# Kernel optimization log

Measured on AMD Instinct MI355X. Metric: run time of the kernel, lower is better.

The kernel has to match this reference:

```python
import jax, jax.numpy as jnp
import numpy as np
import math

CH_IN = 256
NUM_HEADS = 4
HEAD_CH = 64
NUM_GROUPS = 32
EPS = 1e-5


def setup_inputs() -> dict:
    key = jax.random.key(0)
    ks = jax.random.split(key, 12)
    B, C, H, W = 16, CH_IN, 32, 32
    s_in = 1.0 / math.sqrt(C)  # conv 1x1 fan_in init scale
    s_proj = 1.0 / math.sqrt(NUM_HEADS * HEAD_CH)
    return {
        "x": jax.random.normal(ks[0], (B, C, H, W), dtype=jnp.float32),
        "gamma": jnp.ones((C,), dtype=jnp.float32),
        "beta": jnp.zeros((C,), dtype=jnp.float32),
        # per-head 1x1 convs stacked: [num_heads, head_ch, ch_in]
        "wq": jax.random.normal(ks[1], (NUM_HEADS, HEAD_CH, C), dtype=jnp.float32) * s_in,
        "bq": jax.random.normal(ks[2], (NUM_HEADS, HEAD_CH), dtype=jnp.float32) * s_in,
        "wk": jax.random.normal(ks[3], (NUM_HEADS, HEAD_CH, C), dtype=jnp.float32) * s_in,
        "bk": jax.random.normal(ks[4], (NUM_HEADS, HEAD_CH), dtype=jnp.float32) * s_in,
        "wv": jax.random.normal(ks[5], (NUM_HEADS, HEAD_CH, C), dtype=jnp.float32) * s_in,
        "bv": jax.random.normal(ks[6], (NUM_HEADS, HEAD_CH), dtype=jnp.float32) * s_in,
        # output 1x1 conv: [ch_in, num_heads*head_ch]
        "wproj": jax.random.normal(ks[7], (C, NUM_HEADS * HEAD_CH), dtype=jnp.float32) * s_proj,
        "bproj": jax.random.normal(ks[8], (C,), dtype=jnp.float32) * s_proj,
    }


def group_norm(x, gamma, beta):
    B, C, H, W = x.shape
    xg = x.reshape(B, NUM_GROUPS, C // NUM_GROUPS, H, W)
    mean = xg.mean(axis=(2, 3, 4), keepdims=True)
    var = xg.var(axis=(2, 3, 4), keepdims=True)
    xn = (xg - mean) * jax.lax.rsqrt(var + EPS)
    xn = xn.reshape(B, C, H, W)
    return xn * gamma[None, :, None, None] + beta[None, :, None, None]


def reference(x, gamma, beta, wq, bq, wk, bk, wv, bv, wproj, bproj):
    B, C, H, W = x.shape
    L = H * W
    h = group_norm(x, gamma, beta)
    hf = h.reshape(B, C, L)  # [B, C, L]
    # per-head 1x1 convs as batched channel contractions: [B, n_heads, d, L]
    q = jnp.einsum("bcl,ndc->bndl", hf, wq) + bq[None, :, :, None]
    k = jnp.einsum("bcl,ndc->bndl", hf, wk) + bk[None, :, :, None]
    v = jnp.einsum("bcl,ndc->bndl", hf, wv) + bv[None, :, :, None]
    scale = 1.0 / math.sqrt(HEAD_CH)
    scores = jnp.einsum("bndl,bndm->bnlm", q, k) * scale  # [B, n, L, L]
    attn = jax.nn.softmax(scores, axis=-1)
    out = jnp.einsum("bnlm,bndm->bndl", attn, v)  # [B, n, d, L]
    out = out.reshape(B, NUM_HEADS * HEAD_CH, L)  # concat heads along channels
    proj = jnp.einsum("bel,ce->bcl", out, wproj) + bproj[None, :, None]
    return proj.reshape(B, C, H, W) + x
```

## Files before the change

kernel.cpp:

```cpp
#include <hip/hip_runtime.h>
#include <hip/hip_bf16.h>
#include <stdint.h>


typedef __hip_bfloat16 bf16;
typedef __attribute__((ext_vector_type(8))) short short8;
typedef __attribute__((ext_vector_type(4))) float float4v;
typedef __attribute__((ext_vector_type(16))) float float16v;

#if __has_builtin(__builtin_amdgcn_exp2f)
#define EXP2F(x) __builtin_amdgcn_exp2f(x)
#else
#define EXP2F(x) exp2f(x)
#endif

__device__ __forceinline__ float max3f(float a, float b, float c) {
  return fmaxf(fmaxf(a, b), c);
}

__device__ __forceinline__ int qk_fidx(int d, int l) {
  return ((((l >> 5) * 4 + (d >> 4)) * 64 + ((d >> 3) & 1) * 32 + (l & 31)) << 3) + (d & 7);
}
__device__ __forceinline__ int v_fidx(int d, int l) {
  return (((((((l >> 5) * 2 + (d >> 5)) * 2 + ((l >> 4) & 1)) * 2 + ((l >> 3) & 1)) * 32) + (d & 31)) << 3) + (l & 7);
}

__global__ __launch_bounds__(256) void stats_kernel(const float* __restrict__ x,
    float2* __restrict__ stats) {
  int b = blockIdx.x >> 5, g = blockIdx.x & 31;
  const float* xp = x + (size_t)(b * 256 + g * 8) * 1024;
  float s = 0.f, ss = 0.f;
  for (int i = threadIdx.x; i < 8192; i += 256) {
    float v = xp[i]; s += v; ss += v * v;
  }
  #pragma unroll
  for (int o = 32; o; o >>= 1) { s += __shfl_down(s, o); ss += __shfl_down(ss, o); }
  __shared__ float red[2][4];
  int wid = threadIdx.x >> 6;
  if ((threadIdx.x & 63) == 0) { red[0][wid] = s; red[1][wid] = ss; }
  __syncthreads();
  if (threadIdx.x == 0) {
    s  = red[0][0] + red[0][1] + red[0][2] + red[0][3];
    ss = red[1][0] + red[1][1] + red[1][2] + red[1][3];
    float mean = s * (1.f / 8192.f);
    float var  = ss * (1.f / 8192.f) - mean * mean;
    stats[blockIdx.x] = make_float2(mean, rsqrtf(var + 1e-5f));
  }
}

__global__ __launch_bounds__(256) void gnt_kernel(const float* __restrict__ x,
    const float* __restrict__ gamma, const float* __restrict__ beta,
    const float2* __restrict__ stats, bf16* __restrict__ hT, int b_off) {
  __shared__ float T[64][65];
  int zb = blockIdx.z, b = zb + b_off;
  int c0 = blockIdx.y * 64, l0 = blockIdx.x * 64;
  const float* xb = x + (size_t)b * 262144;
  const float2* st = stats + b * 32;
  int tid = threadIdx.x;
  for (int i = tid; i < 4096; i += 256) {
    int cl = i >> 6, ll = i & 63;
    int c = c0 + cl;
    float2 s2 = st[c >> 3];
    T[cl][ll] = (xb[(size_t)c * 1024 + l0 + ll] - s2.x) * s2.y * gamma[c] + beta[c];
  }
  __syncthreads();
  bf16* hb = hT + (size_t)zb * 262144;
  for (int i = tid; i < 4096; i += 256) {
    int ll = i >> 6, cl = i & 63;
    hb[(size_t)(l0 + ll) * 256 + c0 + cl] = __float2bfloat16(T[cl][ll]);
  }
}

__global__ __launch_bounds__(256) void wpack(const float* __restrict__ wq,
    const float* __restrict__ wk, const float* __restrict__ wv,
    const float* __restrict__ wp, bf16* __restrict__ Wb, bf16* __restrict__ Pb) {
  int i = blockIdx.x * 256 + threadIdx.x;
  if (i < 196608) {
    int r = i >> 8, c = i & 255;
    const float* src = (r < 256) ? wq : (r < 512) ? wk : wv;
    Wb[i] = __float2bfloat16(src[(r & 255) * 256 + c]);
  } else {
    int j = i - 196608;
    Pb[j] = __float2bfloat16(wp[j]);
  }
}

__global__ __launch_bounds__(256) void gemm_qkv_mfma(
    const bf16* __restrict__ hT, const bf16* __restrict__ Wb,
    const float* __restrict__ bq, const float* __restrict__ bk,
    const float* __restrict__ bv,
    bf16* __restrict__ qkv, size_t qkv_bstride) {
  __shared__ bf16 As[128][40];
  __shared__ bf16 Bs[128][40];
  int zb = blockIdx.z;
  int m0 = blockIdx.y * 128, l0 = blockIdx.x * 128;
  const bf16* hb = hT + (size_t)zb * 262144;
  int tid = threadIdx.x, lane = tid & 63, wave = tid >> 6;
  int l16 = lane & 15, quad = lane >> 4;
  int mi0 = (wave & 1) * 4, nj0 = (wave >> 1) * 4;
  float4v acc[4][4];
  #pragma unroll
  for (int i = 0; i < 4; i++)
    #pragma unroll
    for (int j = 0; j < 4; j++) acc[i][j] = (float4v){0.f, 0.f, 0.f, 0.f};

  for (int kc = 0; kc < 8; kc++) {
    __syncthreads();
    #pragma unroll
    for (int it = 0; it < 2; it++) {
      int s = it * 256 + tid;
      int mm = s >> 2, kk = (s & 3) * 8;
      *(short8*)&As[mm][kk] = *(const short8*)&Wb[(size_t)(m0 + mm) * 256 + kc * 32 + kk];
      *(short8*)&Bs[mm][kk] = *(const short8*)&hb[(size_t)(l0 + mm) * 256 + kc * 32 + kk];
    }
    __syncthreads();
    short8 af[4], bfr[4];
    #pragma unroll
    for (int i = 0; i < 4; i++) af[i]  = *(const short8*)&As[(mi0 + i) * 16 + l16][quad * 8];
    #pragma unroll
    for (int j = 0; j < 4; j++) bfr[j] = *(const short8*)&Bs[(nj0 + j) * 16 + l16][quad * 8];
    #pragma unroll
    for (int i = 0; i < 4; i++)
      #pragma unroll
      for (int j = 0; j < 4; j++)
        acc[i][j] = __builtin_amdgcn_mfma_f32_16x16x32_bf16(af[i], bfr[j], acc[i][j], 0, 0, 0);
  }

  bf16* Cp = qkv + (size_t)zb * qkv_bstride;
  int sec = m0 >> 8;
  const float* bptr = (sec == 0) ? bq : (sec == 1) ? bk : bv;
  float osc = (sec == 0) ? 0.125f * 1.4426950408889634f : 1.0f;
  #pragma unroll
  for (int i = 0; i < 4; i++) {
    #pragma unroll
    for (int r = 0; r < 4; r++) {
      int m = m0 + (mi0 + i) * 16 + quad * 4 + r;
      int rr = m & 255;
      float bias = bptr[rr];
      int n = rr >> 6, d = rr & 63;
      if (sec <= 1) {
        bf16* Tp = Cp + sec * 262144 + n * 65536;
        #pragma unroll
        for (int j = 0; j < 4; j++) {
          int l = l0 + (nj0 + j) * 16 + l16;
          Tp[qk_fidx(d, l)] = __float2bfloat16((acc[i][j][r] + bias) * osc);
        }
      } else {
        bf16* Vf = Cp + 524288 + n * 65536;
        #pragma unroll
        for (int j = 0; j < 4; j++) {
          int l = l0 + (nj0 + j) * 16 + l16;
          Vf[v_fidx(d, l)] = __float2bfloat16(acc[i][j][r] + bias);
        }
      }
    }
  }
}

__global__ __launch_bounds__(256) void attn_kernel(
    const bf16* __restrict__ qkv, bf16* __restrict__ oT,
    size_t qkv_bstride, size_t o_bstride) {
  __shared__ __align__(16) float OB[2][2][2176];
  __shared__ float mL[2][2][32], lL[2][2][32];

  int zb, n, gg;
  {
    int f = blockIdx.x + (blockIdx.y << 4) + (blockIdx.z << 6);
    if (gridDim.z == 16) {
      int c = f & 7, r = f >> 3;
      int h = (r >> 4) * 8 + c;
      zb = h >> 2; n = h & 3; gg = r & 15;
    } else {
      zb = blockIdx.z; n = blockIdx.y; gg = blockIdx.x;
    }
  }
  const bf16* base = qkv + (size_t)zb * qkv_bstride;
  const bf16* Qf = base + n * 65536;
  const bf16* Kf = base + 262144 + n * 65536;
  const bf16* Vf = base + 524288 + n * 65536;
  int tid = threadIdx.x;
  int lane = tid & 63, wave = tid >> 6;
  int l31 = lane & 31, hb2 = lane >> 5;
  int qt = wave >> 1, half = wave & 1;
  int g = gg * 2 + qt;
  int q0 = g << 5;

  short8 qb[4];
  #pragma unroll
  for (int ds = 0; ds < 4; ds++)
    qb[ds] = *(const short8*)&Qf[(((g * 4 + ds) << 6) + lane) << 3];

  float m_run = -1e30f, l_run = 0.f;
  float16v oaccT[2];
  #pragma unroll
  for (int dh = 0; dh < 2; dh++)
    #pragma unroll
    for (int r = 0; r < 16; r++) oaccT[dh][r] = 0.f;

  auto swp = [&](unsigned int a, unsigned int b, unsigned int& o0, unsigned int& o1) {
#if __has_builtin(__builtin_amdgcn_permlane32_swap)
    auto rr = __builtin_amdgcn_permlane32_swap((int)a, (int)b, false, false);
    o0 = (unsigned int)rr[0]; o1 = (unsigned int)rr[1];
#else
    unsigned int sa = (unsigned int)__shfl_xor((int)a, 32, 64);
    unsigned int sb = (unsigned int)__shfl_xor((int)b, 32, 64);
    o0 = hb2 ? sb : a;
    o1 = hb2 ? b : sa;
#endif
  };

  int k0 = half << 4;
  for (int kt = k0; kt < k0 + 16; kt++) {
    short8 kf[4];
    #pragma unroll
    for (int ds = 0; ds < 4; ds++)
      kf[ds] = *(const short8*)&Kf[(((kt * 4 + ds) << 6) + lane) << 3];
    short8 vf[2][2];
    #pragma unroll
    for (int dh = 0; dh < 2; dh++)
      #pragma unroll
      for (int s = 0; s < 2; s++)
        vf[dh][s] = *(const short8*)&Vf[((((kt * 2 + dh) * 2 + s) << 6) + lane) << 3];

    float16v sacc;
    #pragma unroll
    for (int r = 0; r < 16; r++) sacc[r] = 0.f;
    #pragma unroll
    for (int ds = 0; ds < 4; ds++)
      sacc = __builtin_amdgcn_mfma_f32_32x32x16_bf16(kf[ds], qb[ds], sacc, 0, 0, 0);

    float a0 = max3f(sacc[0], sacc[1], sacc[2]);
    float a1 = max3f(sacc[3], sacc[4], sacc[5]);
    float a2 = max3f(sacc[6], sacc[7], sacc[8]);
    float a3 = max3f(sacc[9], sacc[10], sacc[11]);
    float a4 = max3f(sacc[12], sacc[13], sacc[14]);
    float cmax = fmaxf(max3f(a0, a1, a2), max3f(a3, a4, sacc[15]));
    cmax = fmaxf(cmax, __shfl_xor(cmax, 32, 64));

    if (__any(cmax > m_run + 8.f)) {
      float mnew = fmaxf(m_run, cmax);
      float alpha = EXP2F(m_run - mnew);
      #pragma unroll
      for (int dh = 0; dh < 2; dh++)
        #pragma unroll
        for (int r = 0; r < 16; r++) oaccT[dh][r] *= alpha;
      l_run *= alpha;
      m_run = mnew;
    }

    float p[16];
    #pragma unroll
    for (int r = 0; r < 16; r++) p[r] = EXP2F(sacc[r] - m_run);
    float s0 = (p[0] + p[1]) + (p[2] + p[3]);
    float s1 = (p[4] + p[5]) + (p[6] + p[7]);
    float s2 = (p[8] + p[9]) + (p[10] + p[11]);
    float s3 = (p[12] + p[13]) + (p[14] + p[15]);
    float psum = (s0 + s1) + (s2 + s3);
    psum += __shfl_xor(psum, 32, 64);
    l_run += psum;

    unsigned int w[8];
    #pragma unroll
    for (int i = 0; i < 8; i++) {
      unsigned int pk;
      asm("v_cvt_pk_bf16_f32 %0, %1, %2" : "=v"(pk) : "v"(p[2 * i]), "v"(p[2 * i + 1]));
      w[i] = pk;
    }
    short8 pb[2];
    {
      unsigned int o0, o1, o2, o3;
      swp(w[0], w[2], o0, o2); swp(w[1], w[3], o1, o3);
      unsigned int* pw = (unsigned int*)&pb[0];
      pw[0] = o0; pw[1] = o1; pw[2] = o2; pw[3] = o3;
      swp(w[4], w[6], o0, o2); swp(w[5], w[7], o1, o3);
      pw = (unsigned int*)&pb[1];
      pw[0] = o0; pw[1] = o1; pw[2] = o2; pw[3] = o3;
    }

    #pragma unroll
    for (int dh = 0; dh < 2; dh++)
      #pragma unroll
      for (int s = 0; s < 2; s++)
        oaccT[dh] = __builtin_amdgcn_mfma_f32_32x32x16_bf16(vf[dh][s], pb[s], oaccT[dh], 0, 0, 0);
  }

  #pragma unroll
  for (int dh = 0; dh < 2; dh++)
    #pragma unroll
    for (int rq = 0; rq < 4; rq++) {
      float4v t = {oaccT[dh][4 * rq], oaccT[dh][4 * rq + 1],
                   oaccT[dh][4 * rq + 2], oaccT[dh][4 * rq + 3]};
      *(float4v*)&OB[half][qt][l31 * 68 + dh * 32 + 8 * rq + 4 * hb2] = t;
    }
  if (hb2 == 0) { mL[half][qt][l31] = m_run; lL[half][qt][l31] = l_run; }
  __syncthreads();

  bf16* op = oT + (size_t)zb * o_bstride + n * 64;
  const float* OA = OB[0][qt];
  const float* OBp = OB[1][qt];
  #pragma unroll
  for (int i = 0; i < 16; i++) {
    int q = (half << 4) + i;
    float mA = mL[0][qt][q], mB = mL[1][qt][q];
    float lA = lL[0][qt][q], lB = lL[1][qt][q];
    float ms = fmaxf(mA, mB);
    float eA = EXP2F(mA - ms), eB = EXP2F(mB - ms);
    float inv = 1.f / (lA * eA + lB * eB);
    float va = OA[q * 68 + lane], vb = OBp[q * 68 + lane];
    float o = (va * eA + vb * eB) * inv;
    op[(size_t)(q0 + q) * 256 + lane] = __float2bfloat16(o);
  }
}

__global__ __launch_bounds__(256) void gemm_proj_mfma(
    const bf16* __restrict__ Pb, const bf16* __restrict__ oT,
    const float* __restrict__ bproj, const float* __restrict__ x,
    float* __restrict__ out, int b_off, size_t o_bstride) {
  __shared__ bf16 As[128][40];
  __shared__ bf16 Bs[128][40];
  int zb = blockIdx.z, b = zb + b_off;
  int m0 = blockIdx.y * 128, l0 = blockIdx.x * 128;
  const bf16* ob = oT + (size_t)zb * o_bstride;
  int tid = threadIdx.x, lane = tid & 63, wave = tid >> 6;
  int l16 = lane & 15, quad = lane >> 4;
  int mi0 = (wave & 1) * 4, nj0 = (wave >> 1) * 4;
  float4v acc[4][4];
  #pragma unroll
  for (int i = 0; i < 4; i++)
    #pragma unroll
    for (int j = 0; j < 4; j++) acc[i][j] = (float4v){0.f, 0.f, 0.f, 0.f};

  for (int kc = 0; kc < 8; kc++) {
    __syncthreads();
    #pragma unroll
    for (int it = 0; it < 2; it++) {
      int s = it * 256 + tid;
      int mm = s >> 2, kk = (s & 3) * 8;
      *(short8*)&As[mm][kk] = *(const short8*)&Pb[(size_t)(m0 + mm) * 256 + kc * 32 + kk];
      *(short8*)&Bs[mm][kk] = *(const short8*)&ob[(size_t)(l0 + mm) * 256 + kc * 32 + kk];
    }
    __syncthreads();
    short8 af[4], bfr[4];
    #pragma unroll
    for (int i = 0; i < 4; i++) af[i]  = *(const short8*)&As[(mi0 + i) * 16 + l16][quad * 8];
    #pragma unroll
    for (int j = 0; j < 4; j++) bfr[j] = *(const short8*)&Bs[(nj0 + j) * 16 + l16][quad * 8];
    #pragma unroll
    for (int i = 0; i < 4; i++)
      #pragma unroll
      for (int j = 0; j < 4; j++)
        acc[i][j] = __builtin_amdgcn_mfma_f32_16x16x32_bf16(af[i], bfr[j], acc[i][j], 0, 0, 0);
  }

  #pragma unroll
  for (int i = 0; i < 4; i++) {
    #pragma unroll
    for (int r = 0; r < 4; r++) {
      int m = m0 + (mi0 + i) * 16 + quad * 4 + r;
      float bias = bproj[m];
      #pragma unroll
      for (int j = 0; j < 4; j++) {
        int l = l0 + (nj0 + j) * 16 + l16;
        size_t idx = (size_t)(b * 256 + m) * 1024 + l;
        out[idx] = acc[i][j][r] + bias + x[idx];
      }
    }
  }
}

extern "C" void kernel_launch(void* const* d_in, const int* in_sizes, int n_in,
                              void* d_out, int out_size, void* d_ws, size_t ws_size,
                              hipStream_t stream) {
  int ix = 0, iga = 1, ibe = 2, iwq = 3, ibq = 4, iwk = 5, ibk = 6,
      iwv = 7, ibv = 8, iwp = 9, ibp = 10;
  if (in_sizes[0] != 4194304) {
    if (in_sizes[10] == 4194304 && in_sizes[1] == 256) {
      ibe = 0; ibk = 1; ibp = 2; ibq = 3; ibv = 4; iga = 5;
      iwk = 6; iwp = 7; iwq = 8; iwv = 9; ix = 10;
    } else if (in_sizes[10] == 4194304 && in_sizes[1] == 65536) {
      ibp = 0; iwp = 1; ibv = 2; iwv = 3; ibk = 4; iwk = 5;
      ibq = 6; iwq = 7; ibe = 8; iga = 9; ix = 10;
    } else {
      for (int i = 0; i < 11; i++) if (in_sizes[i] == 4194304) ix = i;
    }
  }
  const float* x     = (const float*)d_in[ix];
  const float* gamma = (const float*)d_in[iga];
  const float* beta  = (const float*)d_in[ibe];
  const float* wq    = (const float*)d_in[iwq];
  const float* bq    = (const float*)d_in[ibq];
  const float* wk    = (const float*)d_in[iwk];
  const float* bk    = (const float*)d_in[ibk];
  const float* wv    = (const float*)d_in[iwv];
  const float* bv    = (const float*)d_in[ibv];
  const float* wproj = (const float*)d_in[iwp];
  const float* bproj = (const float*)d_in[ibp];
  float* out = (float*)d_out;

  const size_t QKV_B = (size_t)768 * 1024;
  const size_t O_B   = (size_t)256 * 1024;
  char* wsp = (char*)d_ws;
  float2* stats = (float2*)wsp;
  bf16* Wb = (bf16*)(wsp + 8192);
  bf16* Pb = (bf16*)(wsp + 8192 + 393216);
  const size_t HT0 = 8192 + 393216 + 131072;
  size_t full_need = HT0 + (size_t)16 * O_B * 2 + (size_t)16 * QKV_B * 2;

  stats_kernel<<<512, 256, 0, stream>>>(x, stats);
  wpack<<<1024, 256, 0, stream>>>(wq, wk, wv, wproj, Wb, Pb);

  if (ws_size >= full_need) {
    bf16* hT  = (bf16*)(wsp + HT0);
    bf16* qkv = (bf16*)(wsp + HT0 + 16 * O_B * 2);
    bf16* oT  = hT;
    gnt_kernel   <<<dim3(16, 4, 16), 256, 0, stream>>>(x, gamma, beta, stats, hT, 0);
    gemm_qkv_mfma<<<dim3(8, 6, 16), 256, 0, stream>>>(hT, Wb, bq, bk, bv, qkv, QKV_B);
    attn_kernel  <<<dim3(16, 4, 16), 256, 0, stream>>>(qkv, oT, QKV_B, O_B);
    gemm_proj_mfma<<<dim3(8, 2, 16), 256, 0, stream>>>(Pb, oT, bproj, x, out, 0, O_B);
  } else {
    bf16* hT  = (bf16*)(wsp + HT0);
    bf16* qkv = (bf16*)(wsp + HT0 + O_B * 2);
    bf16* oT  = hT;
    for (int b = 0; b < 16; b++) {
      gnt_kernel   <<<dim3(16, 4, 1), 256, 0, stream>>>(x, gamma, beta, stats, hT, b);
      gemm_qkv_mfma<<<dim3(8, 6, 1), 256, 0, stream>>>(hT, Wb, bq, bk, bv, qkv, 0);
      attn_kernel  <<<dim3(16, 4, 1), 256, 0, stream>>>(qkv, oT, 0, 0);
      gemm_proj_mfma<<<dim3(8, 2, 1), 256, 0, stream>>>(Pb, oT, bproj, x, out, b, 0);
    }
  }
}
```

Baseline: 179.0 us.

## Fuse GroupNorm into QKV GEMM and merge stats with weight packing

Removes the separate GroupNorm-transpose kernel: the QKV GEMM now reads fp32 x directly, applies per-channel scale/shift from precomputed stats, converts to bf16 and writes the transposed tile into LDS. The stats and weight-packing kernels are merged into one launch. Q/K epilogue stores are packed as four bf16 values per 8-byte write. This saves one launch and the hT round trip through memory. In exchange each of the six M-blocks re-reads and re-normalizes the same x tile, and the LDS transpose writes are scalar.

```diff
diff --git a/kernel.cpp b/kernel.cpp
--- a/kernel.cpp
+++ b/kernel.cpp
@@ -25,79 +25,67 @@
   return (((((((l >> 5) * 2 + (d >> 5)) * 2 + ((l >> 4) & 1)) * 2 + ((l >> 3) & 1)) * 32) + (d & 31)) << 3) + (l & 7);
 }
 
-__global__ __launch_bounds__(256) void stats_kernel(const float* __restrict__ x,
-    float2* __restrict__ stats) {
-  int b = blockIdx.x >> 5, g = blockIdx.x & 31;
-  const float* xp = x + (size_t)(b * 256 + g * 8) * 1024;
-  float s = 0.f, ss = 0.f;
-  for (int i = threadIdx.x; i < 8192; i += 256) {
-    float v = xp[i]; s += v; ss += v * v;
-  }
-  #pragma unroll
-  for (int o = 32; o; o >>= 1) { s += __shfl_down(s, o); ss += __shfl_down(ss, o); }
-  __shared__ float red[2][4];
-  int wid = threadIdx.x >> 6;
-  if ((threadIdx.x & 63) == 0) { red[0][wid] = s; red[1][wid] = ss; }
-  __syncthreads();
-  if (threadIdx.x == 0) {
-    s  = red[0][0] + red[0][1] + red[0][2] + red[0][3];
-    ss = red[1][0] + red[1][1] + red[1][2] + red[1][3];
-    float mean = s * (1.f / 8192.f);
-    float var  = ss * (1.f / 8192.f) - mean * mean;
-    stats[blockIdx.x] = make_float2(mean, rsqrtf(var + 1e-5f));
-  }
-}
-
-__global__ __launch_bounds__(256) void gnt_kernel(const float* __restrict__ x,
-    const float* __restrict__ gamma, const float* __restrict__ beta,
-    const float2* __restrict__ stats, bf16* __restrict__ hT, int b_off) {
-  __shared__ float T[64][65];
-  int zb = blockIdx.z, b = zb + b_off;
-  int c0 = blockIdx.y * 64, l0 = blockIdx.x * 64;
-  const float* xb = x + (size_t)b * 262144;
-  const float2* st = stats + b * 32;
-  int tid = threadIdx.x;
-  for (int i = tid; i < 4096; i += 256) {
-    int cl = i >> 6, ll = i & 63;
-    int c = c0 + cl;
-    float2 s2 = st[c >> 3];
-    T[cl][ll] = (xb[(size_t)c * 1024 + l0 + ll] - s2.x) * s2.y * gamma[c] + beta[c];
-  }
-  __syncthreads();
-  bf16* hb = hT + (size_t)zb * 262144;
-  for (int i = tid; i < 4096; i += 256) {
-    int ll = i >> 6, cl = i & 63;
-    hb[(size_t)(l0 + ll) * 256 + c0 + cl] = __float2bfloat16(T[cl][ll]);
-  }
-}
-
-__global__ __launch_bounds__(256) void wpack(const float* __restrict__ wq,
-    const float* __restrict__ wk, const float* __restrict__ wv,
-    const float* __restrict__ wp, bf16* __restrict__ Wb, bf16* __restrict__ Pb) {
-  int i = blockIdx.x * 256 + threadIdx.x;
-  if (i < 196608) {
-    int r = i >> 8, c = i & 255;
-    const float* src = (r < 256) ? wq : (r < 512) ? wk : wv;
-    Wb[i] = __float2bfloat16(src[(r & 255) * 256 + c]);
+__global__ __launch_bounds__(256) void stats_wpack_kernel(
+    const float* __restrict__ x, float2* __restrict__ stats,
+    const float* __restrict__ wq, const float* __restrict__ wk,
+    const float* __restrict__ wv, const float* __restrict__ wp,
+    bf16* __restrict__ Wb, bf16* __restrict__ Pb) {
+  if (blockIdx.x < 512) {
+    int b = blockIdx.x >> 5, g = blockIdx.x & 31;
+    const float* xp = x + (size_t)(b * 256 + g * 8) * 1024;
+    float s = 0.f, ss = 0.f;
+    for (int i = threadIdx.x; i < 8192; i += 256) {
+      float v = xp[i]; s += v; ss += v * v;
+    }
+    #pragma unroll
+    for (int o = 32; o; o >>= 1) { s += __shfl_down(s, o); ss += __shfl_down(ss, o); }
+    __shared__ float red[2][4];
+    int wid = threadIdx.x >> 6;
+    if ((threadIdx.x & 63) == 0) { red[0][wid] = s; red[1][wid] = ss; }
+    __syncthreads();
+    if (threadIdx.x == 0) {
+      s  = red[0][0] + red[0][1] + red[0][2] + red[0][3];
+      ss = red[1][0] + red[1][1] + red[1][2] + red[1][3];
+      float mean = s * (1.f / 8192.f);
+      float var  = ss * (1.f / 8192.f) - mean * mean;
+      stats[blockIdx.x] = make_float2(mean, rsqrtf(var + 1e-5f));
+    }
   } else {
-    int j = i - 196608;
-    Pb[j] = __float2bfloat16(wp[j]);
-  }
-}
-
-__global__ __launch_bounds__(256) void gemm_qkv_mfma(
-    const bf16* __restrict__ hT, const bf16* __restrict__ Wb,
+    int i = (blockIdx.x - 512) * 256 + threadIdx.x;
+    if (i < 196608) {
+      int r = i >> 8, c = i & 255;
+      const float* src = (r < 256) ? wq : (r < 512) ? wk : wv;
+      Wb[i] = __float2bfloat16(src[(r & 255) * 256 + c]);
+    } else {
+      int j = i - 196608;
+      Pb[j] = __float2bfloat16(wp[j]);
+    }
+  }
+}
+
+__global__ __launch_bounds__(256) void gemm_qkv_fused(
+    const float* __restrict__ x, const float* __restrict__ gamma,
+    const float* __restrict__ beta, const float2* __restrict__ stats,
+    const bf16* __restrict__ Wb,
     const float* __restrict__ bq, const float* __restrict__ bk,
     const float* __restrict__ bv,
-    bf16* __restrict__ qkv, size_t qkv_bstride) {
+    bf16* __restrict__ qkv, size_t qkv_bstride, int b_off) {
   __shared__ bf16 As[128][40];
   __shared__ bf16 Bs[128][40];
-  int zb = blockIdx.z;
+  __shared__ float2 ssh[256];
+  int zb = blockIdx.z, b = zb + b_off;
   int m0 = blockIdx.y * 128, l0 = blockIdx.x * 128;
-  const bf16* hb = hT + (size_t)zb * 262144;
+  const float* xb = x + (size_t)b * 262144;
   int tid = threadIdx.x, lane = tid & 63, wave = tid >> 6;
   int l16 = lane & 15, quad = lane >> 4;
   int mi0 = (wave & 1) * 4, nj0 = (wave >> 1) * 4;
+
+  {
+    float2 st = stats[b * 32 + (tid >> 3)];
+    float sc = st.y * gamma[tid];
+    ssh[tid] = make_float2(sc, beta[tid] - st.x * sc);
+  }
+
   float4v acc[4][4];
   #pragma unroll
   for (int i = 0; i < 4; i++)
@@ -111,7 +99,14 @@
       int s = it * 256 + tid;
       int mm = s >> 2, kk = (s & 3) * 8;
       *(short8*)&As[mm][kk] = *(const short8*)&Wb[(size_t)(m0 + mm) * 256 + kc * 32 + kk];
-      *(short8*)&Bs[mm][kk] = *(const short8*)&hb[(size_t)(l0 + mm) * 256 + kc * 32 + kk];
+    }
+    #pragma unroll
+    for (int it = 0; it < 16; it++) {
+      int i = it * 256 + tid;
+      int cl = i >> 7, ll = i & 127;
+      float2 sh = ssh[kc * 32 + cl];
+      float v = xb[(size_t)(kc * 32 + cl) * 1024 + l0 + ll];
+      Bs[ll][cl] = __float2bfloat16(v * sh.x + sh.y);
     }
     __syncthreads();
     short8 af[4], bfr[4];
@@ -129,31 +124,46 @@
   bf16* Cp = qkv + (size_t)zb * qkv_bstride;
   int sec = m0 >> 8;
   const float* bptr = (sec == 0) ? bq : (sec == 1) ? bk : bv;
-  float osc = (sec == 0) ? 0.125f * 1.4426950408889634f : 1.0f;
-  #pragma unroll
-  for (int i = 0; i < 4; i++) {
-    #pragma unroll
-    for (int r = 0; r < 4; r++) {
-      int m = m0 + (mi0 + i) * 16 + quad * 4 + r;
-      int rr = m & 255;
-      float bias = bptr[rr];
-      int n = rr >> 6, d = rr & 63;
-      if (sec <= 1) {
-        bf16* Tp = Cp + sec * 262144 + n * 65536;
+  if (sec <= 1) {
+    float osc = (sec == 0) ? 0.125f * 1.4426950408889634f : 1.0f;
+    bf16* Tp = Cp + sec * 262144;
+    #pragma unroll
+    for (int i = 0; i < 4; i++) {
+      int rrb = (m0 & 255) + (mi0 + i) * 16 + quad * 4;
+      int nh = rrb >> 6, d0 = rrb & 63;
+      float b0 = bptr[rrb], b1 = bptr[rrb + 1], b2 = bptr[rrb + 2], b3 = bptr[rrb + 3];
+      bf16* Tph = Tp + nh * 65536;
+      #pragma unroll
+      for (int j = 0; j < 4; j++) {
+        int l = l0 + (nj0 + j) * 16 + l16;
+        bf16 h0 = __float2bfloat16((acc[i][j][0] + b0) * osc);
+        bf16 h1 = __float2bfloat16((acc[i][j][1] + b1) * osc);
+        bf16 h2 = __float2bfloat16((acc[i][j][2] + b2) * osc);
+        bf16 h3 = __float2bfloat16((acc[i][j][3] + b3) * osc);
+        uint2 pk;
+        pk.x = (unsigned int)*(unsigned short*)&h0 |
+               ((unsigned int)*(unsigned short*)&h1 << 16);
+        pk.y = (unsigned int)*(unsigned short*)&h2 |
+               ((unsigned int)*(unsigned short*)&h3 << 16);
+        *(uint2*)&Tph[qk_fidx(d0, l)] = pk;
+      }
+    }
+  } else {
+    bf16* Vfp = Cp + 524288;
+    #pragma unroll
+    for (int i = 0; i < 4; i++)
+      #pragma unroll
+      for (int r = 0; r < 4; r++) {
+        int rr = (m0 & 255) + (mi0 + i) * 16 + quad * 4 + r;
+        float bias = bptr[rr];
+        int nh = rr >> 6, d = rr & 63;
+        bf16* Vfh = Vfp + nh * 65536;
         #pragma unroll
         for (int j = 0; j < 4; j++) {
           int l = l0 + (nj0 + j) * 16 + l16;
-          Tp[qk_fidx(d, l)] = __float2bfloat16((acc[i][j][r] + bias) * osc);
-        }
-      } else {
-        bf16* Vf = Cp + 524288 + n * 65536;
-        #pragma unroll
-        for (int j = 0; j < 4; j++) {
-          int l = l0 + (nj0 + j) * 16 + l16;
-          Vf[v_fidx(d, l)] = __float2bfloat16(acc[i][j][r] + bias);
+          Vfh[v_fidx(d, l)] = __float2bfloat16(acc[i][j][r] + bias);
         }
       }
-    }
   }
 }
 
@@ -403,28 +413,25 @@
   float2* stats = (float2*)wsp;
   bf16* Wb = (bf16*)(wsp + 8192);
   bf16* Pb = (bf16*)(wsp + 8192 + 393216);
-  const size_t HT0 = 8192 + 393216 + 131072;
-  size_t full_need = HT0 + (size_t)16 * O_B * 2 + (size_t)16 * QKV_B * 2;
-
-  stats_kernel<<<512, 256, 0, stream>>>(x, stats);
-  wpack<<<1024, 256, 0, stream>>>(wq, wk, wv, wproj, Wb, Pb);
+  const size_t OT0 = 8192 + 393216 + 131072;
+  size_t full_need = OT0 + (size_t)16 * O_B * 2 + (size_t)16 * QKV_B * 2;
+
+  stats_wpack_kernel<<<1536, 256, 0, stream>>>(x, stats, wq, wk, wv, wproj, Wb, Pb);
 
   if (ws_size >= full_need) {
-    bf16* hT  = (bf16*)(wsp + HT0);
-    bf16* qkv = (bf16*)(wsp + HT0 + 16 * O_B * 2);
-    bf16* oT  = hT;
-    gnt_kernel   <<<dim3(16, 4, 16), 256, 0, stream>>>(x, gamma, beta, stats, hT, 0);
-    gemm_qkv_mfma<<<dim3(8, 6, 16), 256, 0, stream>>>(hT, Wb, bq, bk, bv, qkv, QKV_B);
-    attn_kernel  <<<dim3(16, 4, 16), 256, 0, stream>>>(qkv, oT, QKV_B, O_B);
+    bf16* oT  = (bf16*)(wsp + OT0);
+    bf16* qkv = (bf16*)(wsp + OT0 + 16 * O_B * 2);
+    gemm_qkv_fused<<<dim3(8, 6, 16), 256, 0, stream>>>(x, gamma, beta, stats, Wb,
+                                                       bq, bk, bv, qkv, QKV_B, 0);
+    attn_kernel   <<<dim3(16, 4, 16), 256, 0, stream>>>(qkv, oT, QKV_B, O_B);
     gemm_proj_mfma<<<dim3(8, 2, 16), 256, 0, stream>>>(Pb, oT, bproj, x, out, 0, O_B);
   } else {
-    bf16* hT  = (bf16*)(wsp + HT0);
-    bf16* qkv = (bf16*)(wsp + HT0 + O_B * 2);
-    bf16* oT  = hT;
+    bf16* oT  = (bf16*)(wsp + OT0);
+    bf16* qkv = (bf16*)(wsp + OT0 + O_B * 2);
     for (int b = 0; b < 16; b++) {
-      gnt_kernel   <<<dim3(16, 4, 1), 256, 0, stream>>>(x, gamma, beta, stats, hT, b);
-      gemm_qkv_mfma<<<dim3(8, 6, 1), 256, 0, stream>>>(hT, Wb, bq, bk, bv, qkv, 0);
-      attn_kernel  <<<dim3(16, 4, 1), 256, 0, stream>>>(qkv, oT, 0, 0);
+      gemm_qkv_fused<<<dim3(8, 6, 1), 256, 0, stream>>>(x, gamma, beta, stats, Wb,
+                                                        bq, bk, bv, qkv, 0, b);
+      attn_kernel   <<<dim3(16, 4, 1), 256, 0, stream>>>(qkv, oT, 0, 0);
       gemm_proj_mfma<<<dim3(8, 2, 1), 256, 0, stream>>>(Pb, oT, bproj, x, out, b, 0);
     }
   }
```

Result: faster. 174.8 us (-2.4%).
